# Kernel optimization log

Hardware: AMD Instinct MI355X
Metric: run time of the kernel (lower is better)

## Reference

```python
import jax, jax.numpy as jnp
import numpy as np

TOKENS = 8192
MODEL_DIM = 4096
NUM_EXPERTS = 64
K = 2


def setup_inputs() -> dict:
    key = jax.random.key(0)
    kx, kw = jax.random.split(key)
    x = jax.random.normal(kx, (TOKENS, MODEL_DIM), dtype=jnp.float32)
    # nn.Linear default init: U(-1/sqrt(fan_in), 1/sqrt(fan_in)); weight shape [E, D]
    bound = 1.0 / np.sqrt(MODEL_DIM)
    W = jax.random.uniform(kw, (NUM_EXPERTS, MODEL_DIM), dtype=jnp.float32,
                           minval=-bound, maxval=bound)
    return {"x": x, "W": W}


def reference(x, W):
    # TopKGate.forward with k=2, eval mode (no noise): logits -> top2gating
    logits = jnp.einsum("td,ed->te", x.astype(jnp.float32), W)  # [T, E]
    # topk indices (sorted by value, like torch.topk)
    _, topi = jax.lax.top_k(logits, K)                           # [T, K]
    gates = jax.nn.softmax(logits, axis=-1)                      # [T, E]
    # (gates * one_hot(idx)).sum(-1) == gather of gates at idx
    g = jnp.take_along_axis(gates, topi, axis=-1)                # [T, K]
    eps = jnp.finfo(gates.dtype).eps
    denom = jnp.maximum(jnp.sum(g, axis=-1, keepdims=True), eps)
    g = g / denom
    # matches return ([idx1, idx2], [gate1, gate2]) with flattened indices
    return (topi[:, 0], topi[:, 1], g[:, 0], g[:, 1])
```

## Files before the change

kernel.cpp:

```cpp
#include <hip/hip_runtime.h>
#include <float.h>
#include <math.h>

#define TOKENS 8192
#define DIM    4096

typedef _Float16 v8h  __attribute__((ext_vector_type(8)));
typedef float    v4f  __attribute__((ext_vector_type(4)));

typedef __attribute__((address_space(3))) unsigned int lds_uint;
typedef const __attribute__((address_space(1))) unsigned int glob_uint;

__device__ __forceinline__ void stage16(const _Float16* g, _Float16* l) {
    __builtin_amdgcn_global_load_lds((glob_uint*)g, (lds_uint*)l, 16, 0, 0);
}

__global__ __launch_bounds__(256) void prep_w_kernel(
    const float* __restrict__ W, _Float16* __restrict__ WF) {
    int n = blockIdx.x * 256 + threadIdx.x;
    int chunk = n >> 8;
    int et    = (n >> 6) & 3;
    int lane  = n & 63;
    int e  = et * 16 + (lane & 15);
    int k0 = chunk * 32 + (lane >> 4) * 8;
    const float* src = W + (size_t)e * DIM + k0;
    v8h h, l;
    #pragma unroll
    for (int j = 0; j < 8; ++j) {
        float w = src[j];
        _Float16 wh = (_Float16)w;
        h[j] = wh;
        l[j] = (_Float16)((w - (float)wh) * 2048.0f);
    }
    size_t base = (size_t)chunk * 4096 + (size_t)et * 512 + (size_t)lane * 8;
    *(v8h*)(WF + base)        = h;
    *(v8h*)(WF + base + 2048) = l;
}

#define LOAD_A(Aa, Ab, cc) do {                                               \
    const float* ap_ = abase + (cc) * 32;                                     \
    Aa = *(const v4f*)ap_;                                                    \
    Ab = *(const v4f*)(ap_ + 4);                                              \
} while (0)

#define STAGE(BI, cc) stage16(sbase + (size_t)(cc) * 4096, &buf[BI][wq * 512])

#define CVT1(f, j) {                                                          \
    _Float16 h_ = (_Float16)(f);                                              \
    ah[j] = h_;                                                               \
    al[j] = (_Float16)(((f) - (float)h_) * 2048.0f);                          \
}
#define CVT(Aa, Ab) do {                                                      \
    CVT1(Aa[0], 0) CVT1(Aa[1], 1) CVT1(Aa[2], 2) CVT1(Aa[3], 3)               \
    CVT1(Ab[0], 4) CVT1(Ab[1], 5) CVT1(Ab[2], 6) CVT1(Ab[3], 7)               \
} while (0)

#define MFMA16(a, b, c) __builtin_amdgcn_mfma_f32_16x16x32_f16(a, b, c, 0, 0, 0)

#define COMPC(BI, Aa, Ab) do {                                                \
    CVT(Aa, Ab);                                                              \
    const _Float16* bp_ = &buf[BI][0] + (size_t)lane * 8;                     \
    v8h h0_ = *(const v8h*)(bp_);                                             \
    v8h h1_ = *(const v8h*)(bp_ + 512);                                       \
    v8h h2_ = *(const v8h*)(bp_ + 1024);                                      \
    v8h h3_ = *(const v8h*)(bp_ + 1536);                                      \
    v8h l0_ = *(const v8h*)(bp_ + 2048);                                      \
    v8h l1_ = *(const v8h*)(bp_ + 2560);                                      \
    v8h l2_ = *(const v8h*)(bp_ + 3072);                                      \
    v8h l3_ = *(const v8h*)(bp_ + 3584);                                      \
    acc1[0] = MFMA16(ah, h0_, acc1[0]);                                       \
    acc1[1] = MFMA16(ah, h1_, acc1[1]);                                       \
    acc1[2] = MFMA16(ah, h2_, acc1[2]);                                       \
    acc1[3] = MFMA16(ah, h3_, acc1[3]);                                       \
    acc2[0] = MFMA16(al, h0_, acc2[0]);  acc2[0] = MFMA16(ah, l0_, acc2[0]);  \
    acc2[1] = MFMA16(al, h1_, acc2[1]);  acc2[1] = MFMA16(ah, l1_, acc2[1]);  \
    acc2[2] = MFMA16(al, h2_, acc2[2]);  acc2[2] = MFMA16(ah, l2_, acc2[2]);  \
    acc2[3] = MFMA16(al, h3_, acc2[3]);  acc2[3] = MFMA16(ah, l3_, acc2[3]);  \
} while (0)

#define BARRIER_KEEP(n) do {                                                  \
    __builtin_amdgcn_sched_barrier(0);                                        \
    asm volatile("s_waitcnt vmcnt(" #n ")" ::: "memory");                     \
    __builtin_amdgcn_sched_barrier(0);                                        \
    __builtin_amdgcn_s_barrier();                                             \
    __builtin_amdgcn_sched_barrier(0);                                        \
} while (0)

#define ITER_FULL(c, ACa, ACb, ALa, ALb, BCUR, BNXT) do {                     \
    STAGE(BNXT, (c) + 2);                                                     \
    LOAD_A(ALa, ALb, (c) + 2);                                                \
    COMPC(BCUR, ACa, ACb);                                                    \
    BARRIER_KEEP(5);                                                          \
} while (0)

__global__ __launch_bounds__(512, 4) void logits_kernel(
    const float* __restrict__ x,
    const _Float16* __restrict__ WF,
    float* __restrict__ P) {

    __shared__ _Float16 buf[3][4096];

    const int tid  = threadIdx.x;
    const int wq   = tid >> 6;
    const int lane = tid & 63;
    const int kg   = (int)(blockIdx.x & 7);
    const int tg   = (int)(blockIdx.x >> 3);
    const int tok0 = tg * 128 + wq * 16;
    const int art  = lane & 15;
    const int akg  = lane >> 4;
    const int chunk0 = kg * 16;

    const float*    abase = x  + (size_t)(tok0 + art) * DIM + chunk0 * 32 + akg * 8;
    const _Float16* sbase = WF + (size_t)chunk0 * 4096 + (size_t)tid * 8;

    v4f acc1[4], acc2[4];
    #pragma unroll
    for (int e4 = 0; e4 < 4; ++e4) { acc1[e4] = (v4f)0.0f; acc2[e4] = (v4f)0.0f; }

    v4f A0a, A0b, A1a, A1b, A2a, A2b;
    v8h ah, al;

    STAGE(0, 0);
    LOAD_A(A0a, A0b, 0);
    LOAD_A(A1a, A1b, 1);
    STAGE(1, 1);
    BARRIER_KEEP(5);

    ITER_FULL(0,  A0a, A0b, A2a, A2b, 0, 2);
    ITER_FULL(1,  A1a, A1b, A0a, A0b, 1, 0);
    ITER_FULL(2,  A2a, A2b, A1a, A1b, 2, 1);
    ITER_FULL(3,  A0a, A0b, A2a, A2b, 0, 2);
    ITER_FULL(4,  A1a, A1b, A0a, A0b, 1, 0);
    ITER_FULL(5,  A2a, A2b, A1a, A1b, 2, 1);
    ITER_FULL(6,  A0a, A0b, A2a, A2b, 0, 2);
    ITER_FULL(7,  A1a, A1b, A0a, A0b, 1, 0);
    ITER_FULL(8,  A2a, A2b, A1a, A1b, 2, 1);
    ITER_FULL(9,  A0a, A0b, A2a, A2b, 0, 2);
    ITER_FULL(10, A1a, A1b, A0a, A0b, 1, 0);
    ITER_FULL(11, A2a, A2b, A1a, A1b, 2, 1);
    ITER_FULL(12, A0a, A0b, A2a, A2b, 0, 2);
    ITER_FULL(13, A1a, A1b, A0a, A0b, 1, 0);
    COMPC(2, A2a, A2b);
    BARRIER_KEEP(2);
    COMPC(0, A0a, A0b);

    const float inv2048 = 1.0f / 2048.0f;
    #pragma unroll
    for (int e4 = 0; e4 < 4; ++e4) {
        #pragma unroll
        for (int r = 0; r < 4; ++r) {
            float v = acc1[e4][r] + acc2[e4][r] * inv2048;
            P[((size_t)kg * TOKENS + tok0 + akg * 4 + r) * 64 + e4 * 16 + art] = v;
        }
    }
}

__global__ __launch_bounds__(256) void reduce_topk_kernel(
    const float* __restrict__ P, float* __restrict__ out) {
    const int wq   = threadIdx.x >> 6;
    const int lane = threadIdx.x & 63;
    #pragma unroll
    for (int tt = 0; tt < 4; ++tt) {
        int gt = blockIdx.x * 16 + wq * 4 + tt;
        float v = 0.f;
        #pragma unroll
        for (int kg = 0; kg < 8; ++kg)
            v += P[((size_t)kg * TOKENS + gt) * 64 + lane];

        float bv = v; int bi = lane;
        #pragma unroll
        for (int off = 32; off >= 1; off >>= 1) {
            float ov = __shfl_xor(bv, off);
            int   oi = __shfl_xor(bi, off);
            if (ov > bv || (ov == bv && oi < bi)) { bv = ov; bi = oi; }
        }
        float v2 = (lane == bi) ? -FLT_MAX : v;
        float bv2 = v2; int bi2 = lane;
        #pragma unroll
        for (int off = 32; off >= 1; off >>= 1) {
            float ov = __shfl_xor(bv2, off);
            int   oi = __shfl_xor(bi2, off);
            if (ov > bv2 || (ov == bv2 && oi < bi2)) { bv2 = ov; bi2 = oi; }
        }

        if (lane == 0) {
            float g0 = 1.0f / (1.0f + expf(bv2 - bv));
            out[gt]              = (float)bi;
            out[TOKENS + gt]     = (float)bi2;
            out[2 * TOKENS + gt] = g0;
            out[3 * TOKENS + gt] = 1.0f - g0;
        }
    }
}

extern "C" void kernel_launch(void* const* d_in, const int* in_sizes, int n_in,
                              void* d_out, int out_size, void* d_ws, size_t ws_size,
                              hipStream_t stream) {
    const float* x = (const float*)d_in[0];
    const float* W = (const float*)d_in[1];
    float* out     = (float*)d_out;
    _Float16* WF   = (_Float16*)d_ws;
    float* P       = (float*)((char*)d_ws + (1 << 20));

    prep_w_kernel<<<128, 256, 0, stream>>>(W, WF);
    logits_kernel<<<512, 512, 0, stream>>>(x, WF, P);
    reduce_topk_kernel<<<512, 256, 0, stream>>>(P, out);
}
```

Before: 40.61 us.

## Batch activation loads four chunks at a time with deeper prefetch schedule

Replaces the per-chunk rolling A-load pipeline with batched loads of four k-chunks (eight 16-byte loads) into two alternating register sets, prefetching 4-8 chunks ahead. Waitcnt values are adjusted for the new mix of outstanding global loads and LDS stages. The LDS B reads are split into two halves to shorten register live ranges. This deepens memory latency hiding for x at the cost of many more VGPRs, which may hurt occupancy under the 4-wave launch bound. The P workspace offset is also moved to 2 MB.

Measured after the change: 47.61 us. 1.17x slower.

```diff
diff --git a/kernel.cpp b/kernel.cpp
--- a/kernel.cpp
+++ b/kernel.cpp
@@ -37,10 +37,12 @@
     *(v8h*)(WF + base + 2048) = l;
 }
 
-#define LOAD_A(Aa, Ab, cc) do {                                               \
+#define LOAD_A8(S0a, S0b, S1a, S1b, S2a, S2b, S3a, S3b, cc) do {              \
     const float* ap_ = abase + (cc) * 32;                                     \
-    Aa = *(const v4f*)ap_;                                                    \
-    Ab = *(const v4f*)(ap_ + 4);                                              \
+    S0a = *(const v4f*)(ap_);        S0b = *(const v4f*)(ap_ + 4);            \
+    S1a = *(const v4f*)(ap_ + 32);   S1b = *(const v4f*)(ap_ + 36);           \
+    S2a = *(const v4f*)(ap_ + 64);   S2b = *(const v4f*)(ap_ + 68);           \
+    S3a = *(const v4f*)(ap_ + 96);   S3b = *(const v4f*)(ap_ + 100);          \
 } while (0)
 
 #define STAGE(BI, cc) stage16(sbase + (size_t)(cc) * 4096, &buf[BI][wq * 512])
@@ -60,22 +62,26 @@
 #define COMPC(BI, Aa, Ab) do {                                                \
     CVT(Aa, Ab);                                                              \
     const _Float16* bp_ = &buf[BI][0] + (size_t)lane * 8;                     \
-    v8h h0_ = *(const v8h*)(bp_);                                             \
-    v8h h1_ = *(const v8h*)(bp_ + 512);                                       \
-    v8h h2_ = *(const v8h*)(bp_ + 1024);                                      \
-    v8h h3_ = *(const v8h*)(bp_ + 1536);                                      \
-    v8h l0_ = *(const v8h*)(bp_ + 2048);                                      \
-    v8h l1_ = *(const v8h*)(bp_ + 2560);                                      \
-    v8h l2_ = *(const v8h*)(bp_ + 3072);                                      \
-    v8h l3_ = *(const v8h*)(bp_ + 3584);                                      \
-    acc1[0] = MFMA16(ah, h0_, acc1[0]);                                       \
-    acc1[1] = MFMA16(ah, h1_, acc1[1]);                                       \
-    acc1[2] = MFMA16(ah, h2_, acc1[2]);                                       \
-    acc1[3] = MFMA16(ah, h3_, acc1[3]);                                       \
-    acc2[0] = MFMA16(al, h0_, acc2[0]);  acc2[0] = MFMA16(ah, l0_, acc2[0]);  \
-    acc2[1] = MFMA16(al, h1_, acc2[1]);  acc2[1] = MFMA16(ah, l1_, acc2[1]);  \
-    acc2[2] = MFMA16(al, h2_, acc2[2]);  acc2[2] = MFMA16(ah, l2_, acc2[2]);  \
-    acc2[3] = MFMA16(al, h3_, acc2[3]);  acc2[3] = MFMA16(ah, l3_, acc2[3]);  \
+    {                                                                         \
+        v8h h0_ = *(const v8h*)(bp_);                                         \
+        v8h h1_ = *(const v8h*)(bp_ + 512);                                   \
+        v8h l0_ = *(const v8h*)(bp_ + 2048);                                  \
+        v8h l1_ = *(const v8h*)(bp_ + 2560);                                  \
+        acc1[0] = MFMA16(ah, h0_, acc1[0]);                                   \
+        acc1[1] = MFMA16(ah, h1_, acc1[1]);                                   \
+        acc2[0] = MFMA16(al, h0_, acc2[0]);  acc2[0] = MFMA16(ah, l0_, acc2[0]); \
+        acc2[1] = MFMA16(al, h1_, acc2[1]);  acc2[1] = MFMA16(ah, l1_, acc2[1]); \
+    }                                                                         \
+    {                                                                         \
+        v8h h2_ = *(const v8h*)(bp_ + 1024);                                  \
+        v8h h3_ = *(const v8h*)(bp_ + 1536);                                  \
+        v8h l2_ = *(const v8h*)(bp_ + 3072);                                  \
+        v8h l3_ = *(const v8h*)(bp_ + 3584);                                  \
+        acc1[2] = MFMA16(ah, h2_, acc1[2]);                                   \
+        acc1[3] = MFMA16(ah, h3_, acc1[3]);                                   \
+        acc2[2] = MFMA16(al, h2_, acc2[2]);  acc2[2] = MFMA16(ah, l2_, acc2[2]); \
+        acc2[3] = MFMA16(al, h3_, acc2[3]);  acc2[3] = MFMA16(ah, l3_, acc2[3]); \
+    }                                                                         \
 } while (0)
 
 #define BARRIER_KEEP(n) do {                                                  \
@@ -84,13 +90,6 @@
     __builtin_amdgcn_sched_barrier(0);                                        \
     __builtin_amdgcn_s_barrier();                                             \
     __builtin_amdgcn_sched_barrier(0);                                        \
-} while (0)
-
-#define ITER_FULL(c, ACa, ACb, ALa, ALb, BCUR, BNXT) do {                     \
-    STAGE(BNXT, (c) + 2);                                                     \
-    LOAD_A(ALa, ALb, (c) + 2);                                                \
-    COMPC(BCUR, ACa, ACb);                                                    \
-    BARRIER_KEEP(5);                                                          \
 } while (0)
 
 __global__ __launch_bounds__(512, 4) void logits_kernel(
@@ -117,32 +116,36 @@
     #pragma unroll
     for (int e4 = 0; e4 < 4; ++e4) { acc1[e4] = (v4f)0.0f; acc2[e4] = (v4f)0.0f; }
 
-    v4f A0a, A0b, A1a, A1b, A2a, A2b;
+    v4f AP0a, AP0b, AP1a, AP1b, AP2a, AP2b, AP3a, AP3b;
+    v4f AQ0a, AQ0b, AQ1a, AQ1b, AQ2a, AQ2b, AQ3a, AQ3b;
     v8h ah, al;
 
     STAGE(0, 0);
-    LOAD_A(A0a, A0b, 0);
-    LOAD_A(A1a, A1b, 1);
+    LOAD_A8(AP0a, AP0b, AP1a, AP1b, AP2a, AP2b, AP3a, AP3b, 0);
+    LOAD_A8(AQ0a, AQ0b, AQ1a, AQ1b, AQ2a, AQ2b, AQ3a, AQ3b, 4);
     STAGE(1, 1);
-    BARRIER_KEEP(5);
-
-    ITER_FULL(0,  A0a, A0b, A2a, A2b, 0, 2);
-    ITER_FULL(1,  A1a, A1b, A0a, A0b, 1, 0);
-    ITER_FULL(2,  A2a, A2b, A1a, A1b, 2, 1);
-    ITER_FULL(3,  A0a, A0b, A2a, A2b, 0, 2);
-    ITER_FULL(4,  A1a, A1b, A0a, A0b, 1, 0);
-    ITER_FULL(5,  A2a, A2b, A1a, A1b, 2, 1);
-    ITER_FULL(6,  A0a, A0b, A2a, A2b, 0, 2);
-    ITER_FULL(7,  A1a, A1b, A0a, A0b, 1, 0);
-    ITER_FULL(8,  A2a, A2b, A1a, A1b, 2, 1);
-    ITER_FULL(9,  A0a, A0b, A2a, A2b, 0, 2);
-    ITER_FULL(10, A1a, A1b, A0a, A0b, 1, 0);
-    ITER_FULL(11, A2a, A2b, A1a, A1b, 2, 1);
-    ITER_FULL(12, A0a, A0b, A2a, A2b, 0, 2);
-    ITER_FULL(13, A1a, A1b, A0a, A0b, 1, 0);
-    COMPC(2, A2a, A2b);
-    BARRIER_KEEP(2);
-    COMPC(0, A0a, A0b);
+    BARRIER_KEEP(17);
+
+    STAGE(2, 2);  COMPC(0, AP0a, AP0b);  BARRIER_KEEP(1);
+    STAGE(0, 3);  COMPC(1, AP1a, AP1b);  BARRIER_KEEP(1);
+    STAGE(1, 4);  COMPC(2, AP2a, AP2b);  BARRIER_KEEP(1);
+    STAGE(2, 5);  COMPC(0, AP3a, AP3b);
+    LOAD_A8(AP0a, AP0b, AP1a, AP1b, AP2a, AP2b, AP3a, AP3b, 8);
+    BARRIER_KEEP(9);
+    STAGE(0, 6);  COMPC(1, AQ0a, AQ0b);  BARRIER_KEEP(9);
+    STAGE(1, 7);  COMPC(2, AQ1a, AQ1b);  BARRIER_KEEP(1);
+    STAGE(2, 8);  COMPC(0, AQ2a, AQ2b);  BARRIER_KEEP(1);
+    STAGE(0, 9);  COMPC(1, AQ3a, AQ3b);
+    LOAD_A8(AQ0a, AQ0b, AQ1a, AQ1b, AQ2a, AQ2b, AQ3a, AQ3b, 12);
+    BARRIER_KEEP(9);
+    STAGE(1, 10); COMPC(2, AP0a, AP0b);  BARRIER_KEEP(9);
+    STAGE(2, 11); COMPC(0, AP1a, AP1b);  BARRIER_KEEP(1);
+    STAGE(0, 12); COMPC(1, AP2a, AP2b);  BARRIER_KEEP(1);
+    STAGE(1, 13); COMPC(2, AP3a, AP3b);  BARRIER_KEEP(1);
+    STAGE(2, 14); COMPC(0, AQ0a, AQ0b);  BARRIER_KEEP(1);
+    STAGE(0, 15); COMPC(1, AQ1a, AQ1b);  BARRIER_KEEP(1);
+    COMPC(2, AQ2a, AQ2b);                BARRIER_KEEP(0);
+    COMPC(0, AQ3a, AQ3b);
 
     const float inv2048 = 1.0f / 2048.0f;
     #pragma unroll
@@ -200,7 +203,7 @@
     const float* W = (const float*)d_in[1];
     float* out     = (float*)d_out;
     _Float16* WF   = (_Float16*)d_ws;
-    float* P       = (float*)((char*)d_ws + (1 << 20));
+    float* P       = (float*)((char*)d_ws + (2 << 20));
 
     prep_w_kernel<<<128, 256, 0, stream>>>(W, WF);
     logits_kernel<<<512, 512, 0, stream>>>(x, WF, P);
```

## Process two K-chunks per pipeline stage to halve barriers in logits GEMM

Applied to the files above, without the earlier changes.

The logits kernel's software pipeline is restructured so each stage stages two 32-wide K chunks of W into LDS and computes both before a barrier, halving the number of block-wide barriers. The LDS buffers are doubled to 3x8192 halves, and x loads are now issued after the compute of the current stage into the same registers. This is meant to cut synchronisation overhead and raise the MFMA work done between barriers. In exchange it uses more LDS per block, which may reduce occupancy, and the x-prefetch distance changes.

Measured after the change: 43.24 us. 1.06x slower.

```diff
diff --git a/kernel.cpp b/kernel.cpp
--- a/kernel.cpp
+++ b/kernel.cpp
@@ -37,13 +37,16 @@
     *(v8h*)(WF + base + 2048) = l;
 }
 
-#define LOAD_A(Aa, Ab, cc) do {                                               \
-    const float* ap_ = abase + (cc) * 32;                                     \
-    Aa = *(const v4f*)ap_;                                                    \
-    Ab = *(const v4f*)(ap_ + 4);                                              \
-} while (0)
-
-#define STAGE(BI, cc) stage16(sbase + (size_t)(cc) * 4096, &buf[BI][wq * 512])
+#define LOAD_A4(A0a, A0b, A1a, A1b, jj) do {                                  \
+    const float* ap_ = abase + (jj) * 32;                                     \
+    A0a = *(const v4f*)(ap_);       A0b = *(const v4f*)(ap_ + 4);             \
+    A1a = *(const v4f*)(ap_ + 32);  A1b = *(const v4f*)(ap_ + 36);            \
+} while (0)
+
+#define STAGE2(BI, jj) do {                                                   \
+    stage16(sbase + (size_t)(jj) * 4096,       &buf[BI][wq * 1024]);          \
+    stage16(sbase + (size_t)(jj) * 4096 + 512, &buf[BI][wq * 1024 + 512]);    \
+} while (0)
 
 #define CVT1(f, j) {                                                          \
     _Float16 h_ = (_Float16)(f);                                              \
@@ -57,9 +60,9 @@
 
 #define MFMA16(a, b, c) __builtin_amdgcn_mfma_f32_16x16x32_f16(a, b, c, 0, 0, 0)
 
-#define COMPC(BI, Aa, Ab) do {                                                \
+#define COMPC(BI, COFF, Aa, Ab) do {                                          \
     CVT(Aa, Ab);                                                              \
-    const _Float16* bp_ = &buf[BI][0] + (size_t)lane * 8;                     \
+    const _Float16* bp_ = &buf[BI][COFF] + (size_t)lane * 8;                  \
     v8h h0_ = *(const v8h*)(bp_);                                             \
     v8h h1_ = *(const v8h*)(bp_ + 512);                                       \
     v8h h2_ = *(const v8h*)(bp_ + 1024);                                      \
@@ -86,11 +89,12 @@
     __builtin_amdgcn_sched_barrier(0);                                        \
 } while (0)
 
-#define ITER_FULL(c, ACa, ACb, ALa, ALb, BCUR, BNXT) do {                     \
-    STAGE(BNXT, (c) + 2);                                                     \
-    LOAD_A(ALa, ALb, (c) + 2);                                                \
-    COMPC(BCUR, ACa, ACb);                                                    \
-    BARRIER_KEEP(5);                                                          \
+#define ITER_FULL(i, BI, BN, Ac0a, Ac0b, Ac1a, Ac1b) do {                     \
+    STAGE2(BN, 2 * (i) + 4);                                                  \
+    COMPC(BI, 0,    Ac0a, Ac0b);                                              \
+    COMPC(BI, 4096, Ac1a, Ac1b);                                              \
+    LOAD_A4(Ac0a, Ac0b, Ac1a, Ac1b, 2 * (i) + 4);                             \
+    BARRIER_KEEP(10);                                                         \
 } while (0)
 
 __global__ __launch_bounds__(512, 4) void logits_kernel(
@@ -98,7 +102,7 @@
     const _Float16* __restrict__ WF,
     float* __restrict__ P) {
 
-    __shared__ _Float16 buf[3][4096];
+    __shared__ _Float16 buf[3][8192];
 
     const int tid  = threadIdx.x;
     const int wq   = tid >> 6;
@@ -111,38 +115,33 @@
     const int chunk0 = kg * 16;
 
     const float*    abase = x  + (size_t)(tok0 + art) * DIM + chunk0 * 32 + akg * 8;
-    const _Float16* sbase = WF + (size_t)chunk0 * 4096 + (size_t)tid * 8;
+    const _Float16* sbase = WF + (size_t)chunk0 * 4096 + wq * 1024 + lane * 8;
 
     v4f acc1[4], acc2[4];
     #pragma unroll
     for (int e4 = 0; e4 < 4; ++e4) { acc1[e4] = (v4f)0.0f; acc2[e4] = (v4f)0.0f; }
 
-    v4f A0a, A0b, A1a, A1b, A2a, A2b;
+    v4f S0c0a, S0c0b, S0c1a, S0c1b;
+    v4f S1c0a, S1c0b, S1c1a, S1c1b;
     v8h ah, al;
 
-    STAGE(0, 0);
-    LOAD_A(A0a, A0b, 0);
-    LOAD_A(A1a, A1b, 1);
-    STAGE(1, 1);
-    BARRIER_KEEP(5);
-
-    ITER_FULL(0,  A0a, A0b, A2a, A2b, 0, 2);
-    ITER_FULL(1,  A1a, A1b, A0a, A0b, 1, 0);
-    ITER_FULL(2,  A2a, A2b, A1a, A1b, 2, 1);
-    ITER_FULL(3,  A0a, A0b, A2a, A2b, 0, 2);
-    ITER_FULL(4,  A1a, A1b, A0a, A0b, 1, 0);
-    ITER_FULL(5,  A2a, A2b, A1a, A1b, 2, 1);
-    ITER_FULL(6,  A0a, A0b, A2a, A2b, 0, 2);
-    ITER_FULL(7,  A1a, A1b, A0a, A0b, 1, 0);
-    ITER_FULL(8,  A2a, A2b, A1a, A1b, 2, 1);
-    ITER_FULL(9,  A0a, A0b, A2a, A2b, 0, 2);
-    ITER_FULL(10, A1a, A1b, A0a, A0b, 1, 0);
-    ITER_FULL(11, A2a, A2b, A1a, A1b, 2, 1);
-    ITER_FULL(12, A0a, A0b, A2a, A2b, 0, 2);
-    ITER_FULL(13, A1a, A1b, A0a, A0b, 1, 0);
-    COMPC(2, A2a, A2b);
-    BARRIER_KEEP(2);
-    COMPC(0, A0a, A0b);
+    STAGE2(0, 0);
+    LOAD_A4(S0c0a, S0c0b, S0c1a, S0c1b, 0);
+    STAGE2(1, 2);
+    LOAD_A4(S1c0a, S1c0b, S1c1a, S1c1b, 2);
+    BARRIER_KEEP(10);
+
+    ITER_FULL(0, 0, 2, S0c0a, S0c0b, S0c1a, S0c1b);
+    ITER_FULL(1, 1, 0, S1c0a, S1c0b, S1c1a, S1c1b);
+    ITER_FULL(2, 2, 1, S0c0a, S0c0b, S0c1a, S0c1b);
+    ITER_FULL(3, 0, 2, S1c0a, S1c0b, S1c1a, S1c1b);
+    ITER_FULL(4, 1, 0, S0c0a, S0c0b, S0c1a, S0c1b);
+    ITER_FULL(5, 2, 1, S1c0a, S1c0b, S1c1a, S1c1b);
+    COMPC(0, 0,    S0c0a, S0c0b);
+    COMPC(0, 4096, S0c1a, S0c1b);
+    BARRIER_KEEP(4);
+    COMPC(1, 0,    S1c0a, S1c0b);
+    COMPC(1, 4096, S1c1a, S1c1b);
 
     const float inv2048 = 1.0f / 2048.0f;
     #pragma unroll
```
